# Optimization experiments

Measured on AMD Instinct MI355X. Metric: run time of the kernel, lower is better.

The kernel has to match this reference:

```python
import jax, jax.numpy as jnp
import numpy as np

D_IN, D_HID, D_OUT, N_EXP, N_TOK = 1024, 4096, 1024, 8, 4096


def setup_inputs() -> dict:
    key = jax.random.key(0)
    ks = jax.random.split(key, 7)
    x = jax.random.normal(ks[0], (N_TOK, D_IN), dtype=jnp.float32)
    s1 = 1.0 / np.sqrt(D_IN).astype(np.float32)
    s2 = 1.0 / np.sqrt(D_HID).astype(np.float32)
    W1 = jax.random.uniform(ks[1], (N_EXP, D_IN, D_HID), jnp.float32, -s1, s1)
    b1 = jax.random.uniform(ks[2], (N_EXP, D_HID), jnp.float32, -s1, s1)
    W2 = jax.random.uniform(ks[3], (N_EXP, D_HID, D_OUT), jnp.float32, -s2, s2)
    b2 = jax.random.uniform(ks[4], (N_EXP, D_OUT), jnp.float32, -s2, s2)
    Wg = jax.random.uniform(ks[5], (D_IN, N_EXP), jnp.float32, -s1, s1)
    bg = jax.random.uniform(ks[6], (N_EXP,), jnp.float32, -s1, s1)
    return {"x": x, "W1": W1, "b1": b1, "W2": W2, "b2": b2,
            "Wg": Wg, "bg": bg, "top_k": 2}


def reference(x, W1, b1, W2, b2, Wg, bg, top_k):
    # Gating: softmax over experts, then top-k and renormalizing softmax.
    gates = jax.nn.softmax(x @ Wg + bg, axis=-1)            # [N, E]
    topk_vals, topk_idx = jax.lax.top_k(gates, top_k)       # [N, k]
    topk_w = jax.nn.softmax(topk_vals, axis=-1)             # [N, k]
    # Dense all-expert MLP (vectorized replacement for per-token Python loop).
    h = jax.nn.relu(jnp.einsum('nd,edh->neh', x, W1) + b1)  # [N, E, H]
    y = jnp.einsum('neh,eho->neo', h, W2) + b2              # [N, E, O]
    # Combine: gather each token's top-k expert outputs, weighted sum.
    sel = jnp.take_along_axis(y, topk_idx[:, :, None], axis=1)  # [N, k, O]
    out = jnp.sum(topk_w[:, :, None] * sel, axis=1)             # [N, O]
    return out
```

## Files before the change

kernel.cpp:

```cpp
#include <hip/hip_runtime.h>
#include <hip/hip_bf16.h>

#define NTOK 4096
#define DIN  1024
#define DHID 4096
#define DOUT 1024
#define NEXP 8
#define TMAX 72

typedef __hip_bfloat16 bf16;
typedef short short8 __attribute__((ext_vector_type(8)));
typedef float floatx4 __attribute__((ext_vector_type(4)));

#define WAIT_VM0 0x0F70

#define WS_XB    0ull
#define WS_W1T   8388608ull
#define WS_W2T   75497472ull
#define WS_H     142606336ull
#define WS_META  209715200ull
#define MO_CNT    0
#define MO_OFF    64
#define MO_TILE_E 128
#define MO_TILE_S 512
#define MO_TILE_R 896
#define MO_NT     1280
#define MO_CURG   1344
#define MO_T2I    1536
#define MO_T2W    34304
#define MO_ROWS   67072
#define MO_ROWW   99840

__device__ __forceinline__ void gload16(const bf16* g, bf16* l) {
  __builtin_amdgcn_global_load_lds(
      (const __attribute__((address_space(1))) void*)g,
      (__attribute__((address_space(3))) void*)l, 16, 0, 0);
}

__global__ void k_cast_x(const float* __restrict__ in, bf16* __restrict__ out) {
  int i = (blockIdx.x * 256 + threadIdx.x) * 8;
  float4 a = *(const float4*)(in + i);
  float4 b = *(const float4*)(in + i + 4);
  union { int4 v; bf16 h[8]; } u;
  u.h[0] = __float2bfloat16(a.x); u.h[1] = __float2bfloat16(a.y);
  u.h[2] = __float2bfloat16(a.z); u.h[3] = __float2bfloat16(a.w);
  u.h[4] = __float2bfloat16(b.x); u.h[5] = __float2bfloat16(b.y);
  u.h[6] = __float2bfloat16(b.z); u.h[7] = __float2bfloat16(b.w);
  *(int4*)(out + i) = u.v;
}

__global__ void k_transpose_cast(const float* __restrict__ in, bf16* __restrict__ out,
                                 int R, int C) {
  __shared__ float t[64][65];
  size_t ebase = (size_t)blockIdx.z * R * C;
  int c0 = blockIdx.x * 64, r0 = blockIdx.y * 64;
  int tid = threadIdx.x;
  int rr = tid >> 4;
  int cq = (tid & 15) * 4;
  #pragma unroll
  for (int i = 0; i < 4; i++) {
    int r = rr + i * 16;
    float4 v = *(const float4*)(in + ebase + (size_t)(r0 + r) * C + c0 + cq);
    t[cq + 0][r] = v.x; t[cq + 1][r] = v.y; t[cq + 2][r] = v.z; t[cq + 3][r] = v.w;
  }
  __syncthreads();
  int cc = tid >> 3;
  int rq = (tid & 7) * 8;
  #pragma unroll
  for (int i = 0; i < 2; i++) {
    int c = cc + i * 32;
    union { int4 v; bf16 h[8]; } u;
    #pragma unroll
    for (int j = 0; j < 8; j++) u.h[j] = __float2bfloat16(t[c][rq + j]);
    *(int4*)(out + ebase + (size_t)(c0 + c) * R + r0 + rq) = u.v;
  }
}

__global__ void k_gate(const float* __restrict__ x, const float* __restrict__ Wg,
                       const float* __restrict__ bg, int* __restrict__ t2i,
                       float* __restrict__ t2w, int* __restrict__ cnt) {
  int wave = threadIdx.x >> 6, lane = threadIdx.x & 63;
  int t = blockIdx.x * 4 + wave;
  const float* xr = x + (size_t)t * DIN;
  float acc[8] = {0.f, 0.f, 0.f, 0.f, 0.f, 0.f, 0.f, 0.f};
  for (int d = lane; d < DIN; d += 64) {
    float xv = xr[d];
    const float* wr = Wg + d * 8;
    float4 w0 = *(const float4*)wr;
    float4 w1 = *(const float4*)(wr + 4);
    acc[0] += xv * w0.x; acc[1] += xv * w0.y; acc[2] += xv * w0.z; acc[3] += xv * w0.w;
    acc[4] += xv * w1.x; acc[5] += xv * w1.y; acc[6] += xv * w1.z; acc[7] += xv * w1.w;
  }
  #pragma unroll
  for (int off = 32; off; off >>= 1) {
    #pragma unroll
    for (int e = 0; e < 8; e++) acc[e] += __shfl_xor(acc[e], off, 64);
  }
  if (lane == 0) {
    float p[8], m = -1e30f, s = 0.f;
    #pragma unroll
    for (int e = 0; e < 8; e++) { p[e] = acc[e] + bg[e]; m = fmaxf(m, p[e]); }
    #pragma unroll
    for (int e = 0; e < 8; e++) { p[e] = expf(p[e] - m); s += p[e]; }
    float inv = 1.f / s;
    #pragma unroll
    for (int e = 0; e < 8; e++) p[e] *= inv;
    int i0 = 0;
    #pragma unroll
    for (int e = 1; e < 8; e++) if (p[e] > p[i0]) i0 = e;
    int i1 = (i0 == 0) ? 1 : 0;
    #pragma unroll
    for (int e = 0; e < 8; e++) if (e != i0 && p[e] > p[i1]) i1 = e;
    float d = expf(p[i1] - p[i0]);
    float w0 = 1.f / (1.f + d), w1 = d / (1.f + d);
    t2i[2 * t] = i0; t2i[2 * t + 1] = i1;
    t2w[2 * t] = w0; t2w[2 * t + 1] = w1;
    atomicAdd(&cnt[i0], 1);
    atomicAdd(&cnt[i1], 1);
  }
}

__global__ void k_meta(const int* __restrict__ cnt, int* __restrict__ off,
                       int* __restrict__ tile_e, int* __restrict__ tile_s,
                       int* __restrict__ tile_r, int* __restrict__ nt,
                       int* __restrict__ cur_g) {
  if (threadIdx.x == 0) {
    int o = 0, n = 0;
    for (int e = 0; e < 8; e++) {
      off[e] = o; cur_g[e] = o;
      int c = cnt[e];
      for (int r = 0; r < c; r += 128) {
        tile_e[n] = e; tile_s[n] = o + r; tile_r[n] = min(128, c - r); n++;
      }
      o += c;
    }
    *nt = n;
  }
}

__global__ void k_scatter(const int* __restrict__ t2i, const float* __restrict__ t2w,
                          int* __restrict__ cur_g, int* __restrict__ rows,
                          float* __restrict__ roww) {
  __shared__ int lcnt[8], lbase[8];
  if (threadIdx.x < 8) lcnt[threadIdx.x] = 0;
  __syncthreads();
  int t = blockIdx.x * 256 + threadIdx.x;
  int e0 = t2i[2 * t], e1 = t2i[2 * t + 1];
  int p0 = atomicAdd(&lcnt[e0], 1);
  int p1 = atomicAdd(&lcnt[e1], 1);
  __syncthreads();
  if (threadIdx.x < 8)
    lbase[threadIdx.x] = atomicAdd(&cur_g[threadIdx.x], lcnt[threadIdx.x]);
  __syncthreads();
  int a0 = lbase[e0] + p0, a1 = lbase[e1] + p1;
  rows[a0] = t; roww[a0] = t2w[2 * t];
  rows[a1] = t; roww[a1] = t2w[2 * t + 1];
}

template <int MODE>
__global__ __launch_bounds__(256)
void k_gemm(const bf16* __restrict__ A, const bf16* __restrict__ Bt,
            const float* __restrict__ bias,
            const int* __restrict__ tile_e, const int* __restrict__ tile_s,
            const int* __restrict__ tile_r, const int* __restrict__ nt,
            const int* __restrict__ rows, const float* __restrict__ roww,
            bf16* __restrict__ hout, float* __restrict__ out,
            int K, int N) {
  int tile = blockIdx.x;
  if (tile >= *nt) return;
  int e = tile_e[tile], start = tile_s[tile], mrows = tile_r[tile];
  int n0 = blockIdx.y * 128;
  int tid = threadIdx.x, lane = tid & 63, wave = tid >> 6;
  int wm = wave & 1, wn = wave >> 1;

  __shared__ bf16 Al[2][128 * 32];
  __shared__ bf16 Bl[2][128 * 32];

  int srow = tid >> 2;
  int kc8  = (tid & 3) * 8;
  int ra0 = srow, ra1 = 64 + srow;
  int er0 = ra0 < mrows ? ra0 : 0;
  int er1 = ra1 < mrows ? ra1 : 0;
  size_t ga0, ga1;
  if (MODE == 1) {
    ga0 = (size_t)rows[start + er0] * K;
    ga1 = (size_t)rows[start + er1] * K;
  } else {
    ga0 = (size_t)(start + er0) * K;
    ga1 = (size_t)(start + er1) * K;
  }
  const bf16* ap0 = A + ga0 + kc8;
  const bf16* ap1 = A + ga1 + kc8;
  const bf16* bb = Bt + (size_t)e * K * N + (size_t)n0 * K;
  const bf16* bp0 = bb + (size_t)srow * K + kc8;
  const bf16* bp1 = bb + (size_t)(64 + srow) * K + kc8;

  floatx4 zz = {0.f, 0.f, 0.f, 0.f};
  floatx4 acc[4][4];
  #pragma unroll
  for (int i = 0; i < 4; i++)
    #pragma unroll
    for (int j = 0; j < 4; j++) acc[i][j] = zz;

  int fr = lane & 15, ko = (lane >> 4) * 8;

  gload16(ap0, &Al[0][tid * 8]);
  gload16(ap1, &Al[0][2048 + tid * 8]);
  gload16(bp0, &Bl[0][tid * 8]);
  gload16(bp1, &Bl[0][2048 + tid * 8]);

  int cur = 0;
  for (int k0 = 0; k0 < K; k0 += 32) {
    __builtin_amdgcn_s_waitcnt(WAIT_VM0);
    __builtin_amdgcn_s_barrier();

    short8 af[4], bfr[4];
    #pragma unroll
    for (int i = 0; i < 4; i++)
      af[i] = *(const short8*)&Al[cur][(wm * 64 + i * 16 + fr) * 32 + ko];
    #pragma unroll
    for (int j = 0; j < 4; j++)
      bfr[j] = *(const short8*)&Bl[cur][(wn * 64 + j * 16 + fr) * 32 + ko];

    int nxt = cur ^ 1;
    if (k0 + 32 < K) {
      gload16(ap0 + k0 + 32, &Al[nxt][tid * 8]);
      gload16(ap1 + k0 + 32, &Al[nxt][2048 + tid * 8]);
      gload16(bp0 + k0 + 32, &Bl[nxt][tid * 8]);
      gload16(bp1 + k0 + 32, &Bl[nxt][2048 + tid * 8]);
    }

    #pragma unroll
    for (int i = 0; i < 4; i++)
      #pragma unroll
      for (int j = 0; j < 4; j++)
        acc[i][j] = __builtin_amdgcn_mfma_f32_16x16x32_bf16(af[i], bfr[j], acc[i][j], 0, 0, 0);
    cur = nxt;
  }

  int col_l = lane & 15, quad = lane >> 4;
  if (MODE == 1) {
    #pragma unroll
    for (int i = 0; i < 4; i++) {
      #pragma unroll
      for (int r = 0; r < 4; r++) {
        int row = wm * 64 + i * 16 + quad * 4 + r;
        if (row < mrows) {
          size_t rb = (size_t)(start + row) * N;
          #pragma unroll
          for (int j = 0; j < 4; j++) {
            int col = n0 + wn * 64 + j * 16 + col_l;
            float v = acc[i][j][r] + bias[e * N + col];
            hout[rb + col] = __float2bfloat16(fmaxf(v, 0.f));
          }
        }
      }
    }
  } else {
    #pragma unroll
    for (int i = 0; i < 4; i++) {
      #pragma unroll
      for (int r = 0; r < 4; r++) {
        int row = wm * 64 + i * 16 + quad * 4 + r;
        if (row < mrows) {
          int tok = rows[start + row];
          float w = roww[start + row];
          size_t ob = (size_t)tok * N;
          #pragma unroll
          for (int j = 0; j < 4; j++) {
            int col = n0 + wn * 64 + j * 16 + col_l;
            float v = (acc[i][j][r] + bias[e * N + col]) * w;
            unsafeAtomicAdd(&out[ob + col], v);
          }
        }
      }
    }
  }
}

extern "C" void kernel_launch(void* const* d_in, const int* in_sizes, int n_in,
                              void* d_out, int out_size, void* d_ws, size_t ws_size,
                              hipStream_t stream) {
  const float* x  = (const float*)d_in[0];
  const float* W1 = (const float*)d_in[1];
  const float* b1 = (const float*)d_in[2];
  const float* W2 = (const float*)d_in[3];
  const float* b2 = (const float*)d_in[4];
  const float* Wg = (const float*)d_in[5];
  const float* bg = (const float*)d_in[6];
  float* out = (float*)d_out;
  char* ws = (char*)d_ws;

  bf16* xb  = (bf16*)(ws + WS_XB);
  bf16* w1t = (bf16*)(ws + WS_W1T);
  bf16* w2t = (bf16*)(ws + WS_W2T);
  bf16* h   = (bf16*)(ws + WS_H);
  char* meta = ws + WS_META;
  int*   cnt    = (int*)(meta + MO_CNT);
  int*   off    = (int*)(meta + MO_OFF);
  int*   tile_e = (int*)(meta + MO_TILE_E);
  int*   tile_s = (int*)(meta + MO_TILE_S);
  int*   tile_r = (int*)(meta + MO_TILE_R);
  int*   nt     = (int*)(meta + MO_NT);
  int*   cur_g  = (int*)(meta + MO_CURG);
  int*   t2i    = (int*)(meta + MO_T2I);
  float* t2w    = (float*)(meta + MO_T2W);
  int*   rows   = (int*)(meta + MO_ROWS);
  float* roww   = (float*)(meta + MO_ROWW);

  hipMemsetAsync(cnt, 0, 64, stream);
  hipMemsetAsync(d_out, 0, (size_t)out_size * sizeof(float), stream);

  k_cast_x<<<(NTOK * DIN) / (256 * 8), 256, 0, stream>>>(x, xb);
  k_transpose_cast<<<dim3(DHID / 64, DIN / 64, NEXP), 256, 0, stream>>>(W1, w1t, DIN, DHID);
  k_transpose_cast<<<dim3(DOUT / 64, DHID / 64, NEXP), 256, 0, stream>>>(W2, w2t, DHID, DOUT);
  k_gate<<<NTOK / 4, 256, 0, stream>>>(x, Wg, bg, t2i, t2w, cnt);
  k_meta<<<1, 64, 0, stream>>>(cnt, off, tile_e, tile_s, tile_r, nt, cur_g);
  k_scatter<<<NTOK / 256, 256, 0, stream>>>(t2i, t2w, cur_g, rows, roww);
  k_gemm<1><<<dim3(TMAX, DHID / 128), 256, 0, stream>>>(
      xb, w1t, b1, tile_e, tile_s, tile_r, nt, rows, roww, h, nullptr, DIN, DHID);
  k_gemm<2><<<dim3(TMAX, DOUT / 128), 256, 0, stream>>>(
      h, w2t, b2, tile_e, tile_s, tile_r, nt, rows, roww, nullptr, out, DHID, DOUT);
}
```

Baseline: 704.8 us.

## Triple-buffer GEMM loads, swizzle LDS, remap tiles to XCDs, fuse x cast into gate

The grouped GEMM moves from double to triple buffering, prefetching two k-steps ahead and waiting with a partial vmcnt so global-to-LDS loads overlap more compute. LDS columns are rotated per row pair to cut bank conflicts on fragment reads. Block IDs are remapped so each XCD handles a contiguous group of tiles, aiming for better L2 reuse of expert weights. The separate x-to-bf16 cast kernel is folded into the gating kernel, dropping one launch and one read of x. The cost is more LDS per block and hardcoded tile-mapping constants (9 tiles per XCD, TMAX=72).

```diff
diff --git a/kernel.cpp b/kernel.cpp
--- a/kernel.cpp
+++ b/kernel.cpp
@@ -10,9 +10,11 @@
 
 typedef __hip_bfloat16 bf16;
 typedef short short8 __attribute__((ext_vector_type(8)));
+typedef short short4v __attribute__((ext_vector_type(4)));
 typedef float floatx4 __attribute__((ext_vector_type(4)));
 
 #define WAIT_VM0 0x0F70
+#define WAIT_VM4 0x0F74
 
 #define WS_XB    0ull
 #define WS_W1T   8388608ull
@@ -37,18 +39,6 @@
       (__attribute__((address_space(3))) void*)l, 16, 0, 0);
 }
 
-__global__ void k_cast_x(const float* __restrict__ in, bf16* __restrict__ out) {
-  int i = (blockIdx.x * 256 + threadIdx.x) * 8;
-  float4 a = *(const float4*)(in + i);
-  float4 b = *(const float4*)(in + i + 4);
-  union { int4 v; bf16 h[8]; } u;
-  u.h[0] = __float2bfloat16(a.x); u.h[1] = __float2bfloat16(a.y);
-  u.h[2] = __float2bfloat16(a.z); u.h[3] = __float2bfloat16(a.w);
-  u.h[4] = __float2bfloat16(b.x); u.h[5] = __float2bfloat16(b.y);
-  u.h[6] = __float2bfloat16(b.z); u.h[7] = __float2bfloat16(b.w);
-  *(int4*)(out + i) = u.v;
-}
-
 __global__ void k_transpose_cast(const float* __restrict__ in, bf16* __restrict__ out,
                                  int R, int C) {
   __shared__ float t[64][65];
@@ -77,19 +67,32 @@
 }
 
 __global__ void k_gate(const float* __restrict__ x, const float* __restrict__ Wg,
-                       const float* __restrict__ bg, int* __restrict__ t2i,
-                       float* __restrict__ t2w, int* __restrict__ cnt) {
+                       const float* __restrict__ bg, bf16* __restrict__ xb,
+                       int* __restrict__ t2i, float* __restrict__ t2w,
+                       int* __restrict__ cnt) {
   int wave = threadIdx.x >> 6, lane = threadIdx.x & 63;
   int t = blockIdx.x * 4 + wave;
   const float* xr = x + (size_t)t * DIN;
+  bf16* xbr = xb + (size_t)t * DIN;
   float acc[8] = {0.f, 0.f, 0.f, 0.f, 0.f, 0.f, 0.f, 0.f};
-  for (int d = lane; d < DIN; d += 64) {
-    float xv = xr[d];
-    const float* wr = Wg + d * 8;
-    float4 w0 = *(const float4*)wr;
-    float4 w1 = *(const float4*)(wr + 4);
-    acc[0] += xv * w0.x; acc[1] += xv * w0.y; acc[2] += xv * w0.z; acc[3] += xv * w0.w;
-    acc[4] += xv * w1.x; acc[5] += xv * w1.y; acc[6] += xv * w1.z; acc[7] += xv * w1.w;
+  #pragma unroll
+  for (int i = 0; i < 4; i++) {
+    int d0 = (lane + i * 64) * 4;
+    float4 v = *(const float4*)(xr + d0);
+    union { short4v s; bf16 h[4]; } u;
+    u.h[0] = __float2bfloat16(v.x); u.h[1] = __float2bfloat16(v.y);
+    u.h[2] = __float2bfloat16(v.z); u.h[3] = __float2bfloat16(v.w);
+    *(short4v*)(xbr + d0) = u.s;
+    float xv4[4] = {v.x, v.y, v.z, v.w};
+    #pragma unroll
+    for (int c = 0; c < 4; c++) {
+      const float* wr = Wg + (size_t)(d0 + c) * 8;
+      float4 w0 = *(const float4*)wr;
+      float4 w1 = *(const float4*)(wr + 4);
+      float xv = xv4[c];
+      acc[0] += xv * w0.x; acc[1] += xv * w0.y; acc[2] += xv * w0.z; acc[3] += xv * w0.w;
+      acc[4] += xv * w1.x; acc[5] += xv * w1.y; acc[6] += xv * w1.z; acc[7] += xv * w1.w;
+    }
   }
   #pragma unroll
   for (int off = 32; off; off >>= 1) {
@@ -166,18 +169,21 @@
             const int* __restrict__ rows, const float* __restrict__ roww,
             bf16* __restrict__ hout, float* __restrict__ out,
             int K, int N) {
-  int tile = blockIdx.x;
+  int hwid = blockIdx.x + blockIdx.y * gridDim.x;
+  int xcd = hwid & 7, pos = hwid >> 3;
+  int tile = xcd * 9 + pos % 9;
   if (tile >= *nt) return;
+  int n0 = (pos / 9) * 128;
   int e = tile_e[tile], start = tile_s[tile], mrows = tile_r[tile];
-  int n0 = blockIdx.y * 128;
   int tid = threadIdx.x, lane = tid & 63, wave = tid >> 6;
   int wm = wave & 1, wn = wave >> 1;
 
-  __shared__ bf16 Al[2][128 * 32];
-  __shared__ bf16 Bl[2][128 * 32];
+  __shared__ bf16 Al[3][128 * 32];
+  __shared__ bf16 Bl[3][128 * 32];
 
   int srow = tid >> 2;
-  int kc8  = (tid & 3) * 8;
+  int rot = (srow >> 1) & 3;
+  int kc8 = (((tid & 3) - rot) & 3) * 8;
   int ra0 = srow, ra1 = 64 + srow;
   int er0 = ra0 < mrows ? ra0 : 0;
   int er1 = ra1 < mrows ? ra1 : 0;
@@ -202,16 +208,25 @@
     #pragma unroll
     for (int j = 0; j < 4; j++) acc[i][j] = zz;
 
-  int fr = lane & 15, ko = (lane >> 4) * 8;
-
-  gload16(ap0, &Al[0][tid * 8]);
-  gload16(ap1, &Al[0][2048 + tid * 8]);
-  gload16(bp0, &Bl[0][tid * 8]);
-  gload16(bp1, &Bl[0][2048 + tid * 8]);
-
+  int fr = lane & 15;
+  int ko = (((lane >> 4) + ((fr >> 1) & 3)) & 3) * 8;
+
+#define STAGE(buf, kk)                                    \
+  do {                                                    \
+    gload16(ap0 + (kk), &Al[buf][tid * 8]);               \
+    gload16(ap1 + (kk), &Al[buf][2048 + tid * 8]);        \
+    gload16(bp0 + (kk), &Bl[buf][tid * 8]);               \
+    gload16(bp1 + (kk), &Bl[buf][2048 + tid * 8]);        \
+  } while (0)
+
+  STAGE(0, 0);
+  STAGE(1, 32);
+
+  int nk = K >> 5;
   int cur = 0;
-  for (int k0 = 0; k0 < K; k0 += 32) {
-    __builtin_amdgcn_s_waitcnt(WAIT_VM0);
+  for (int t = 0; t < nk; ++t) {
+    if (t + 1 < nk) __builtin_amdgcn_s_waitcnt(WAIT_VM4);
+    else            __builtin_amdgcn_s_waitcnt(WAIT_VM0);
     __builtin_amdgcn_s_barrier();
 
     short8 af[4], bfr[4];
@@ -222,12 +237,9 @@
     for (int j = 0; j < 4; j++)
       bfr[j] = *(const short8*)&Bl[cur][(wn * 64 + j * 16 + fr) * 32 + ko];
 
-    int nxt = cur ^ 1;
-    if (k0 + 32 < K) {
-      gload16(ap0 + k0 + 32, &Al[nxt][tid * 8]);
-      gload16(ap1 + k0 + 32, &Al[nxt][2048 + tid * 8]);
-      gload16(bp0 + k0 + 32, &Bl[nxt][tid * 8]);
-      gload16(bp1 + k0 + 32, &Bl[nxt][2048 + tid * 8]);
+    if (t + 2 < nk) {
+      int nb = cur + 2; if (nb >= 3) nb -= 3;
+      STAGE(nb, (t + 2) * 32);
     }
 
     #pragma unroll
@@ -235,8 +247,9 @@
       #pragma unroll
       for (int j = 0; j < 4; j++)
         acc[i][j] = __builtin_amdgcn_mfma_f32_16x16x32_bf16(af[i], bfr[j], acc[i][j], 0, 0, 0);
-    cur = nxt;
-  }
+    cur = (cur + 1 == 3) ? 0 : cur + 1;
+  }
+#undef STAGE
 
   int col_l = lane & 15, quad = lane >> 4;
   if (MODE == 1) {
@@ -311,10 +324,9 @@
   hipMemsetAsync(cnt, 0, 64, stream);
   hipMemsetAsync(d_out, 0, (size_t)out_size * sizeof(float), stream);
 
-  k_cast_x<<<(NTOK * DIN) / (256 * 8), 256, 0, stream>>>(x, xb);
   k_transpose_cast<<<dim3(DHID / 64, DIN / 64, NEXP), 256, 0, stream>>>(W1, w1t, DIN, DHID);
   k_transpose_cast<<<dim3(DOUT / 64, DHID / 64, NEXP), 256, 0, stream>>>(W2, w2t, DHID, DOUT);
-  k_gate<<<NTOK / 4, 256, 0, stream>>>(x, Wg, bg, t2i, t2w, cnt);
+  k_gate<<<NTOK / 4, 256, 0, stream>>>(x, Wg, bg, xb, t2i, t2w, cnt);
   k_meta<<<1, 64, 0, stream>>>(cnt, off, tile_e, tile_s, tile_r, nt, cur_g);
   k_scatter<<<NTOK / 256, 256, 0, stream>>>(t2i, t2w, cur_g, rows, roww);
   k_gemm<1><<<dim3(TMAX, DHID / 128), 256, 0, stream>>>(
```

Result: faster. 672.3 us (-4.6%).
